# Kernel optimization log

Measured on AMD Instinct MI355X. Metric: run time of the kernel, lower is better.

## Reference

```python
import jax, jax.numpy as jnp
import numpy as np

V = 32000      # vocab
TMAX = 1024    # BLOCK_SIZE
D = 768        # N_EMBD
H = 12         # N_HEAD
L = 12         # N_LAYER
HS = D // H    # head_size
FF = 4 * D
B, T = 4, 1024


def setup_inputs() -> dict:
    key = jax.random.key(0)
    ks = iter(jax.random.split(key, 40))
    n = lambda shape: 0.02 * jax.random.normal(next(ks), shape, dtype=jnp.float32)
    return dict(
        idx=jax.random.randint(next(ks), (B, T), 0, V),
        targets=jax.random.randint(next(ks), (B, T), 0, V),
        tok_emb=n((V, D)),
        pos_emb=n((TMAX, D)),
        Wq=n((L, H, D, HS)), Wk=n((L, H, D, HS)), Wv=n((L, H, D, HS)),
        Wo=n((L, D, D)), bo=jnp.zeros((L, D)),
        W1=n((L, D, FF)), b1=jnp.zeros((L, FF)),
        W2=n((L, FF, D)), b2=jnp.zeros((L, D)),
        ln1_g=jnp.ones((L, D)), ln1_b=jnp.zeros((L, D)),
        ln2_g=jnp.ones((L, D)), ln2_b=jnp.zeros((L, D)),
        lnf_g=jnp.ones((D,)), lnf_b=jnp.zeros((D,)),
        Wlm=n((D, V)), blm=jnp.zeros((V,)),
    )


def _ln(x, g, b, eps=1e-5):
    m = x.mean(-1, keepdims=True)
    v = x.var(-1, keepdims=True)
    return (x - m) * jax.lax.rsqrt(v + eps) * g + b


def reference(idx, targets, tok_emb, pos_emb, Wq, Wk, Wv, Wo, bo,
              W1, b1, W2, b2, ln1_g, ln1_b, ln2_g, ln2_b, lnf_g, lnf_b,
              Wlm, blm):
    Bsz, Tt = idx.shape
    x = tok_emb[idx] + pos_emb[:Tt]                      # [B,T,D]
    causal = jnp.tril(jnp.ones((Tt, Tt), dtype=bool))     # [T,T]

    def layer(x, p):
        wq, wk, wv, wo, bob, w1, b1b, w2, b2b, g1, be1, g2, be2 = p
        h = _ln(x, g1, be1)
        q = jnp.einsum('btd,hdk->bhtk', h, wq)
        k = jnp.einsum('btd,hdk->bhtk', h, wk)
        v = jnp.einsum('btd,hdk->bhtk', h, wv)
        wei = jnp.einsum('bhtk,bhsk->bhts', q, k) * (HS ** -0.5)
        wei = jnp.where(causal, wei, -jnp.inf)
        wei = jax.nn.softmax(wei, axis=-1)                # dropout=0 in eval
        att = jnp.einsum('bhts,bhsk->bhtk', wei, v)
        att = att.transpose(0, 2, 1, 3).reshape(Bsz, Tt, H * HS)  # concat heads
        x = x + att @ wo + bob
        h2 = _ln(x, g2, be2)
        x = x + jax.nn.relu(h2 @ w1 + b1b) @ w2 + b2b
        return x, None

    x, _ = jax.lax.scan(layer, x,
                        (Wq, Wk, Wv, Wo, bo, W1, b1, W2, b2,
                         ln1_g, ln1_b, ln2_g, ln2_b))
    x = _ln(x, lnf_g, lnf_b)
    logits = x @ Wlm + blm                                # [B,T,V]
    lf = logits.reshape(Bsz * Tt, V)
    tf = targets.reshape(-1)
    logp = jax.nn.log_softmax(lf, axis=-1)
    loss = -jnp.take_along_axis(logp, tf[:, None], axis=1).mean()
    return lf, loss
```

## Files before the change

kernel.cpp:

```cpp
#include <hip/hip_runtime.h>

constexpr int C_B   = 4;
constexpr int C_T   = 1024;
constexpr int C_D   = 768;
constexpr int C_H   = 12;
constexpr int C_HS  = 64;
constexpr int C_FF  = 3072;
constexpr int C_V   = 32000;
constexpr int C_L   = 12;
constexpr int ROWS  = C_B * C_T;
constexpr int QKVN  = 3 * C_D;

typedef __bf16 bf16;
typedef __attribute__((ext_vector_type(8))) __bf16 bf16x8;
typedef __attribute__((ext_vector_type(4))) float  f32x4;
typedef __attribute__((ext_vector_type(4))) short  s16x4;

static __device__ __forceinline__ void gload16(const void* g, void* l) {
  __builtin_amdgcn_global_load_lds((const __attribute__((address_space(1))) void*)g,
                                   (__attribute__((address_space(3))) void*)l,
                                   16, 0, 0);
}

__global__ __launch_bounds__(256) void embed_kernel(const int* __restrict__ idx,
    const float* __restrict__ tok, const float* __restrict__ pos, float* __restrict__ x) {
  int gid = blockIdx.x * 256 + threadIdx.x;
  int row = gid / C_D, d = gid - row * C_D;
  int t = row & (C_T - 1);
  x[gid] = tok[(long)idx[row] * C_D + d] + pos[(long)t * C_D + d];
}

__global__ __launch_bounds__(256) void ln_kernel(const float* __restrict__ x,
    const float* __restrict__ g, const float* __restrict__ bb, long goff,
    bf16* __restrict__ out) {
  int row = blockIdx.x, tid = threadIdx.x;
  const float* xr = x + (long)row * C_D;
  float v0 = xr[tid], v1 = xr[tid + 256], v2 = xr[tid + 512];
  float s = v0 + v1 + v2;
  float s2 = v0 * v0 + v1 * v1 + v2 * v2;
#pragma unroll
  for (int off = 32; off > 0; off >>= 1) {
    s  += __shfl_down(s, off);
    s2 += __shfl_down(s2, off);
  }
  __shared__ float sm[4], sq[4];
  if ((tid & 63) == 0) { sm[tid >> 6] = s; sq[tid >> 6] = s2; }
  __syncthreads();
  s  = sm[0] + sm[1] + sm[2] + sm[3];
  s2 = sq[0] + sq[1] + sq[2] + sq[3];
  float mean = s * (1.f / C_D);
  float var  = s2 * (1.f / C_D) - mean * mean;
  float rstd = rsqrtf(var + 1e-5f);
  bf16* orow = out + (long)row * C_D;
  orow[tid]       = (bf16)((v0 - mean) * rstd * g[goff + tid]       + bb[goff + tid]);
  orow[tid + 256] = (bf16)((v1 - mean) * rstd * g[goff + tid + 256] + bb[goff + tid + 256]);
  orow[tid + 512] = (bf16)((v2 - mean) * rstd * g[goff + tid + 512] + bb[goff + tid + 512]);
}

__global__ __launch_bounds__(256) void transpose_kernel(const float* __restrict__ src,
    bf16* __restrict__ dst, int K, int N, long soff0, int ntn) {
  __shared__ bf16 tile[32][33];
  const float* s = src + soff0;
  int tn = blockIdx.x % ntn, tk = blockIdx.x / ntn;
  int c = threadIdx.x & 31, r = threadIdx.x >> 5;
#pragma unroll
  for (int it = 0; it < 4; ++it)
    tile[r + 8 * it][c] = (bf16)s[(long)(tk * 32 + r + 8 * it) * N + tn * 32 + c];
  __syncthreads();
#pragma unroll
  for (int it = 0; it < 4; ++it)
    dst[(long)(tn * 32 + r + 8 * it) * K + tk * 32 + c] = tile[c][r + 8 * it];
}

__global__ __launch_bounds__(256) void transpose_layer_kernel(
    const float* __restrict__ Wq, const float* __restrict__ Wk,
    const float* __restrict__ Wv, const float* __restrict__ Wo,
    const float* __restrict__ W1, const float* __restrict__ W2,
    bf16* __restrict__ wqkvt, bf16* __restrict__ wot,
    bf16* __restrict__ w1t, bf16* __restrict__ w2t, int l) {
  int bid = blockIdx.x;
  const float* src; bf16* dst; int K, N, ntn, t;
  if (bid < 1728) {
    int which = bid / 576, r = bid % 576, head = r / 48;
    t = r % 48;
    const float* W = which == 0 ? Wq : which == 1 ? Wk : Wv;
    src = W + (long)l * C_H * C_D * C_HS + (long)head * C_D * C_HS;
    dst = wqkvt + (long)which * C_D * C_D + (long)head * C_HS * C_D;
    K = C_D; N = C_HS; ntn = 2;
  } else if (bid < 2304) {
    t = bid - 1728; src = Wo + (long)l * C_D * C_D; dst = wot;
    K = C_D; N = C_D; ntn = 24;
  } else if (bid < 4608) {
    t = bid - 2304; src = W1 + (long)l * C_D * C_FF; dst = w1t;
    K = C_D; N = C_FF; ntn = 96;
  } else {
    t = bid - 4608; src = W2 + (long)l * C_FF * C_D; dst = w2t;
    K = C_FF; N = C_D; ntn = 24;
  }
  __shared__ bf16 tile[32][33];
  int tn = t % ntn, tk = t / ntn;
  int c = threadIdx.x & 31, r = threadIdx.x >> 5;
#pragma unroll
  for (int it = 0; it < 4; ++it)
    tile[r + 8 * it][c] = (bf16)src[(long)(tk * 32 + r + 8 * it) * N + tn * 32 + c];
  __syncthreads();
#pragma unroll
  for (int it = 0; it < 4; ++it)
    dst[(long)(tn * 32 + r + 8 * it) * K + tk * 32 + c] = tile[c][r + 8 * it];
}

template <int MODE>
__global__ __launch_bounds__(512) void gemm256(const bf16* __restrict__ A,
    const bf16* __restrict__ Bt, const float* __restrict__ bias, long boff,
    void* __restrict__ outp, int N, int K) {
  __shared__ __attribute__((aligned(16))) char smem[131072];
  int tid = threadIdx.x;
  int l = tid & 63, w = tid >> 6;
  int wm = w >> 2, wn = w & 3;
  int lg = l >> 4, lr = l & 15;

  int nwg = gridDim.x;
  int fid = blockIdx.x;
  int swz = (fid & 7) * (nwg >> 3) + (fid >> 3);
  long row0 = (long)(swz & 15) * 256;
  long col0 = (long)(swz >> 4) * 256;

  int Y0 = tid * 16, Y1 = 8192 + tid * 16;
  auto dec = [](int Y, int& R, int& C) {
    int s = Y >> 10, y = Y & 1023;
    int r15 = y >> 6, z = y & 63;
    int q = (z ^ ((r15 & 8) << 2)) >> 4;
    R = (s >> 1) * 16 + r15;
    C = (s & 1) * 32 + q * 8;
  };
  int R0, C0, R1, C1;
  dec(Y0, R0, C0);  dec(Y1, R1, C1);
  const bf16* Ab = A  + row0 * K;
  const bf16* Bb = Bt + col0 * K;

  auto stage = [&](int d, int kt) {
    char* bb = smem + d * 65536;
    long kc = (long)kt * 64;
    gload16(Ab + (long)R0 * K + kc + C0, bb + Y0);
    gload16(Ab + (long)R1 * K + kc + C1, bb + Y1);
    gload16(Ab + (long)(128 + R0) * K + kc + C0, bb + 16384 + Y0);
    gload16(Ab + (long)(128 + R1) * K + kc + C1, bb + 16384 + Y1);
    gload16(Bb + (long)R0 * K + kc + C0, bb + 32768 + Y0);
    gload16(Bb + (long)R1 * K + kc + C1, bb + 32768 + Y1);
    gload16(Bb + (long)(128 + R0) * K + kc + C0, bb + 49152 + Y0);
    gload16(Bb + (long)(128 + R1) * K + kc + C1, bb + 49152 + Y1);
  };

  f32x4 acc[8][4];
  const f32x4 fz = {0.f, 0.f, 0.f, 0.f};
#pragma unroll
  for (int mf = 0; mf < 8; ++mf)
#pragma unroll
    for (int nf = 0; nf < 4; ++nf) acc[mf][nf] = fz;

  int aoff = lr * 64 + ((lg * 16) ^ ((lr & 8) << 2));
  int nk = K >> 6;
  stage(0, 0);
  int d = 0;
  for (int kt = 0; kt < nk; ++kt) {
    __syncthreads();
    if (kt + 1 < nk) stage(d ^ 1, kt + 1);
    const char* aB = smem + d * 65536 + wm * 16384;
    const char* bB = smem + d * 65536 + 32768 + (wn >> 1) * 16384;
    bf16x8 bfrag[4][2];
#pragma unroll
    for (int nf = 0; nf < 4; ++nf)
#pragma unroll
      for (int k = 0; k < 2; ++k)
        bfrag[nf][k] = *(const bf16x8*)(bB + ((((wn & 1) * 4 + nf) * 2 + k) << 10) + aoff);
#pragma unroll
    for (int p = 0; p < 4; ++p) {
      bf16x8 af[2][2];
#pragma unroll
      for (int mi = 0; mi < 2; ++mi)
#pragma unroll
        for (int k = 0; k < 2; ++k)
          af[mi][k] = *(const bf16x8*)(aB + (((p * 2 + mi) * 2 + k) << 10) + aoff);
      __builtin_amdgcn_s_setprio(1);
#pragma unroll
      for (int mi = 0; mi < 2; ++mi)
#pragma unroll
        for (int nf = 0; nf < 4; ++nf)
#pragma unroll
          for (int k = 0; k < 2; ++k)
            acc[p * 2 + mi][nf] = __builtin_amdgcn_mfma_f32_16x16x32_bf16(
                af[mi][k], bfrag[nf][k], acc[p * 2 + mi][nf], 0, 0, 0);
      __builtin_amdgcn_s_setprio(0);
    }
    d ^= 1;
  }
  __syncthreads();

  if (MODE == 0 || MODE == 1) {
    bf16* lc = (bf16*)smem;
#pragma unroll
    for (int nf = 0; nf < 4; ++nf) {
      int col = wn * 64 + nf * 16 + lr;
      float bv = bias ? bias[boff + col0 + col] : 0.f;
#pragma unroll
      for (int mf = 0; mf < 8; ++mf) {
        int rb = wm * 128 + mf * 16 + lg * 4;
#pragma unroll
        for (int r = 0; r < 4; ++r) {
          float v = acc[mf][nf][r] + bv;
          if (MODE == 1) v = fmaxf(v, 0.f);
          lc[(rb + r) * 256 + col] = (bf16)v;
        }
      }
    }
    __syncthreads();
#pragma unroll
    for (int it = 0; it < 16; ++it) {
      int byte = it * 8192 + tid * 16;
      int rl = byte >> 9, cb = byte & 511;
      *(bf16x8*)((bf16*)outp + (row0 + rl) * N + col0 + (cb >> 1)) =
          *(const bf16x8*)(smem + byte);
    }
  } else {
#pragma unroll
    for (int h = 0; h < 2; ++h) {
      if (h) __syncthreads();
      if (wm == h) {
        float* lf = (float*)smem;
#pragma unroll
        for (int nf = 0; nf < 4; ++nf) {
          int col = wn * 64 + nf * 16 + lr;
          float bv = bias ? bias[boff + col0 + col] : 0.f;
#pragma unroll
          for (int mf = 0; mf < 8; ++mf) {
            int rb = mf * 16 + lg * 4;
#pragma unroll
            for (int r = 0; r < 4; ++r)
              lf[(rb + r) * 256 + col] = acc[mf][nf][r] + bv;
          }
        }
      }
      __syncthreads();
#pragma unroll
      for (int it = 0; it < 16; ++it) {
        int byte = it * 8192 + tid * 16;
        int rl = byte >> 10, cb = byte & 1023;
        *(f32x4*)((float*)outp + (row0 + h * 128 + rl) * N + col0 + (cb >> 2)) =
            *(const f32x4*)(smem + byte);
      }
    }
  }
}

template <int MODE>
__global__ __launch_bounds__(256) void gemm_bt(const bf16* __restrict__ A,
    const bf16* __restrict__ Bt, const float* __restrict__ bias, long boff,
    void* __restrict__ outp, float* __restrict__ resid, int N, int K) {
  __shared__ __attribute__((aligned(16))) char smem[32768];
  int tid = threadIdx.x;
  int l = tid & 63;
  int w = tid >> 6, wr = w >> 1, wc = w & 1;
  int lg = l >> 4, lr = l & 15;

  int nwg = gridDim.x;
  int fid = blockIdx.x;
  int swz = (fid & 7) * (nwg >> 3) + (fid >> 3);
  long row0 = (long)(swz & 31) * 128;
  long col0 = (long)(swz >> 5) * 128;

  const bf16* ga = A  + (row0 + (tid >> 2)) * K + (tid & 3) * 8;
  const bf16* gb = Bt + (col0 + (tid >> 2)) * K + (tid & 3) * 8;

  f32x4 acc[4][4];
  const f32x4 fz = {0.f, 0.f, 0.f, 0.f};
#pragma unroll
  for (int m = 0; m < 4; ++m)
#pragma unroll
    for (int n = 0; n < 4; ++n) acc[m][n] = fz;

  int nk = K >> 5;
  {
    bf16* la = (bf16*)smem + tid * 8;
    bf16* lb = (bf16*)(smem + 8192) + tid * 8;
    gload16(ga, la);  gload16(ga + (long)64 * K, la + 2048);
    gload16(gb, lb);  gload16(gb + (long)64 * K, lb + 2048);
    ga += 32; gb += 32;
  }
  int cur = 0;
  for (int t = 0; t < nk; ++t) {
    __syncthreads();
    if (t + 1 < nk) {
      char* bufb = smem + (cur ^ 1) * 16384;
      bf16* la = (bf16*)bufb + tid * 8;
      bf16* lb = (bf16*)(bufb + 8192) + tid * 8;
      gload16(ga, la);  gload16(ga + (long)64 * K, la + 2048);
      gload16(gb, lb);  gload16(gb + (long)64 * K, lb + 2048);
      ga += 32; gb += 32;
    }
    const bf16* cA = (const bf16*)(smem + cur * 16384);
    const bf16* cB = (const bf16*)(smem + cur * 16384 + 8192);
    bf16x8 af[4], bfr[4];
#pragma unroll
    for (int m = 0; m < 4; ++m)
      af[m] = *(const bf16x8*)(cA + (wr * 64 + m * 16 + lr) * 32 + lg * 8);
#pragma unroll
    for (int n = 0; n < 4; ++n)
      bfr[n] = *(const bf16x8*)(cB + (wc * 64 + n * 16 + lr) * 32 + lg * 8);
#pragma unroll
    for (int m = 0; m < 4; ++m)
#pragma unroll
      for (int n = 0; n < 4; ++n)
        acc[m][n] = __builtin_amdgcn_mfma_f32_16x16x32_bf16(af[m], bfr[n], acc[m][n], 0, 0, 0);
    cur ^= 1;
  }
  __syncthreads();

#pragma unroll
  for (int pair = 0; pair < 2; ++pair) {
    float* lcf = (float*)smem;
#pragma unroll
    for (int n = 0; n < 4; ++n) {
      int gcl = wc * 64 + n * 16 + lr;
      float bv = bias ? bias[boff + col0 + gcl] : 0.f;
#pragma unroll
      for (int mi = 0; mi < 2; ++mi) {
        int m = pair * 2 + mi;
        int rl = wr * 32 + mi * 16 + lg * 4;
#pragma unroll
        for (int r = 0; r < 4; ++r)
          lcf[(rl + r) * 128 + gcl] = acc[m][n][r] + bv;
      }
    }
    __syncthreads();
#pragma unroll
    for (int it = 0; it < 8; ++it) {
      int byte = it * 4096 + tid * 16;
      int rl = byte >> 9;
      int cb = byte & 511;
      long gr = row0 + (rl >> 5) * 64 + pair * 32 + ((rl >> 4) & 1) * 16 + (rl & 15);
      f32x4 v = *(const f32x4*)(smem + byte);
      if (MODE == 2) {
        f32x4 g = *(const f32x4*)(resid + gr * N + col0 + (cb >> 2));
        v += g;
        *(f32x4*)(resid + gr * N + col0 + (cb >> 2)) = v;
      } else {
        *(f32x4*)((float*)outp + gr * N + col0 + (cb >> 2)) = v;
      }
    }
    __syncthreads();
  }
}

#define TRRD(D, OFF) asm volatile("ds_read_b64_tr_b16 %0, %1 offset:" OFF \
                                  : "=v"(D) : "v"(trp))
__global__ __launch_bounds__(64) void attn_kernel(const bf16* __restrict__ qkv,
                                                  bf16* __restrict__ attout) {
  int fid = blockIdx.x;
  int swzb = (fid & 7) * 384 + (fid >> 3);
  int qt = swzb & 63;
  int bh = swzb >> 6;
  int b = bh / C_H, h = bh % C_H;
  int l = threadIdx.x;
  int lg = l >> 4, lr = l & 15;
  const bf16* base = qkv + (long)b * C_T * QKVN;

  const bf16* qp = base + (long)(qt * 16 + lr) * QKVN + h * C_HS;
  bf16x8 qf0 = *(const bf16x8*)(qp + lg * 8);
  bf16x8 qf1 = *(const bf16x8*)(qp + 32 + lg * 8);

  const f32x4 fz = {0.f, 0.f, 0.f, 0.f};
  f32x4 o[4] = {fz, fz, fz, fz};
  float m_run[4], l_run[4];
#pragma unroll
  for (int r = 0; r < 4; ++r) { m_run[r] = -1e30f; l_run[r] = 0.f; }

  __shared__ __attribute__((aligned(16))) bf16 p_lds[16][40];
  __shared__ __attribute__((aligned(16))) bf16 vt_sub[2048];

  unsigned trp = (unsigned)(unsigned long)
      ((const __attribute__((address_space(3))) char*)vt_sub + l * 8);

  int nkt = (qt * 16 + 15) / 32 + 1;
  for (int kt = 0; kt < nkt; ++kt) {
    int key0 = kt * 32;
    f32x4 sacc[2];
#pragma unroll
    for (int ss = 0; ss < 2; ++ss) {
      const bf16* kp = base + (long)(key0 + ss * 16 + lr) * QKVN + C_D + h * C_HS;
      bf16x8 kf0 = *(const bf16x8*)(kp + lg * 8);
      bf16x8 kf1 = *(const bf16x8*)(kp + 32 + lg * 8);
      f32x4 a = fz;
      a = __builtin_amdgcn_mfma_f32_16x16x32_bf16(qf0, kf0, a, 0, 0, 0);
      a = __builtin_amdgcn_mfma_f32_16x16x32_bf16(qf1, kf1, a, 0, 0, 0);
      sacc[ss] = a;
    }
#pragma unroll
    for (int r = 0; r < 4; ++r) {
      int qrow = qt * 16 + lg * 4 + r;
      bool u0 = (key0 + lr) <= qrow;
      bool u1 = (key0 + 16 + lr) <= qrow;
      float s0 = u0 ? sacc[0][r] * 0.125f : -1e30f;
      float s1 = u1 ? sacc[1][r] * 0.125f : -1e30f;
      float mr = fmaxf(s0, s1);
      mr = fmaxf(mr, __shfl_xor(mr, 1));
      mr = fmaxf(mr, __shfl_xor(mr, 2));
      mr = fmaxf(mr, __shfl_xor(mr, 4));
      mr = fmaxf(mr, __shfl_xor(mr, 8));
      float mnew = fmaxf(m_run[r], mr);
      float scale = __expf(m_run[r] - mnew);
      float p0 = u0 ? __expf(s0 - mnew) : 0.f;
      float p1 = u1 ? __expf(s1 - mnew) : 0.f;
      float rs = p0 + p1;
      rs += __shfl_xor(rs, 1);
      rs += __shfl_xor(rs, 2);
      rs += __shfl_xor(rs, 4);
      rs += __shfl_xor(rs, 8);
      l_run[r] = l_run[r] * scale + rs;
      m_run[r] = mnew;
      o[0][r] *= scale; o[1][r] *= scale; o[2][r] *= scale; o[3][r] *= scale;
      p_lds[lg * 4 + r][lr]      = (bf16)p0;
      p_lds[lg * 4 + r][16 + lr] = (bf16)p1;
    }
#pragma unroll
    for (int it = 0; it < 4; ++it) {
      int kl = it * 8 + (l >> 3);
      int d0 = (l & 7) * 8;
      bf16x8 vv = *(const bf16x8*)(base + (long)(key0 + kl) * QKVN + 2 * C_D + h * C_HS + d0);
      int ba = ((d0 >> 4) << 10) + (((kl >> 2) & 1) << 9) + ((kl >> 3) << 7)
             + ((kl & 3) << 5) + ((d0 & 15) << 1);
      *(bf16x8*)((char*)vt_sub + ba) = vv;
    }
    __syncthreads();
    s16x4 t0a, t0b, t1a, t1b, t2a, t2b, t3a, t3b;
    TRRD(t0a, "0");    TRRD(t0b, "512");
    TRRD(t1a, "1024"); TRRD(t1b, "1536");
    TRRD(t2a, "2048"); TRRD(t2b, "2560");
    TRRD(t3a, "3072"); TRRD(t3b, "3584");
    bf16x8 pf = *(const bf16x8*)(&p_lds[lr][lg * 8]);
    asm volatile("s_waitcnt lgkmcnt(0)" ::: "memory");
    __builtin_amdgcn_sched_barrier(0);
    union uu { short s[8]; bf16x8 v; };
    auto mk = [](s16x4 a, s16x4 bq) {
      uu u;
      u.s[0] = a[0]; u.s[1] = a[1]; u.s[2] = a[2]; u.s[3] = a[3];
      u.s[4] = bq[0]; u.s[5] = bq[1]; u.s[6] = bq[2]; u.s[7] = bq[3];
      return u.v;
    };
    o[0] = __builtin_amdgcn_mfma_f32_16x16x32_bf16(pf, mk(t0a, t0b), o[0], 0, 0, 0);
    o[1] = __builtin_amdgcn_mfma_f32_16x16x32_bf16(pf, mk(t1a, t1b), o[1], 0, 0, 0);
    o[2] = __builtin_amdgcn_mfma_f32_16x16x32_bf16(pf, mk(t2a, t2b), o[2], 0, 0, 0);
    o[3] = __builtin_amdgcn_mfma_f32_16x16x32_bf16(pf, mk(t3a, t3b), o[3], 0, 0, 0);
    __syncthreads();
  }
#pragma unroll
  for (int c = 0; c < 4; ++c)
#pragma unroll
    for (int r = 0; r < 4; ++r) {
      int qrow = qt * 16 + lg * 4 + r;
      attout[((long)b * C_T + qrow) * C_D + h * C_HS + c * 16 + lr] =
          (bf16)(o[c][r] / l_run[r]);
    }
}

__global__ __launch_bounds__(256) void loss_kernel(const float* __restrict__ logits,
    const int* __restrict__ targets, float* __restrict__ rowloss) {
  int row = blockIdx.x, tid = threadIdx.x;
  const float* lrow = logits + (long)row * C_V;
  float m = -1e30f, sum = 0.f;
  for (int i4 = tid * 4; i4 < C_V; i4 += 1024) {
    f32x4 v4 = *(const f32x4*)(lrow + i4);
#pragma unroll
    for (int j = 0; j < 4; ++j) {
      float v = v4[j];
      if (v > m) { sum *= __expf(m - v); m = v; }
      sum += __expf(v - m);
    }
  }
#pragma unroll
  for (int off = 32; off > 0; off >>= 1) {
    float mo = __shfl_down(m, off), so = __shfl_down(sum, off);
    float M = fmaxf(m, mo);
    sum = sum * __expf(m - M) + so * __expf(mo - M);
    m = M;
  }
  __shared__ float sm[4], ss[4];
  if ((tid & 63) == 0) { sm[tid >> 6] = m; ss[tid >> 6] = sum; }
  __syncthreads();
  if (tid == 0) {
    float M = sm[0], S = ss[0];
    for (int wv = 1; wv < 4; ++wv) {
      float M2 = fmaxf(M, sm[wv]);
      S = S * __expf(M - M2) + ss[wv] * __expf(sm[wv] - M2);
      M = M2;
    }
    float lt = lrow[targets[row]];
    rowloss[row] = -(lt - M - logf(S));
  }
}

__global__ __launch_bounds__(256) void loss_final(const float* __restrict__ rowloss,
                                                  float* __restrict__ out) {
  int tid = threadIdx.x;
  float s = 0.f;
  for (int i = tid; i < ROWS; i += 256) s += rowloss[i];
#pragma unroll
  for (int off = 32; off > 0; off >>= 1) s += __shfl_down(s, off);
  __shared__ float sm[4];
  if ((tid & 63) == 0) sm[tid >> 6] = s;
  __syncthreads();
  if (tid == 0) out[0] = (sm[0] + sm[1] + sm[2] + sm[3]) * (1.f / ROWS);
}

extern "C" void kernel_launch(void* const* d_in, const int* in_sizes, int n_in,
                              void* d_out, int out_size, void* d_ws, size_t ws_size,
                              hipStream_t stream) {
  (void)in_sizes; (void)n_in; (void)out_size; (void)ws_size;
  const int*   idx     = (const int*)  d_in[0];
  const int*   targets = (const int*)  d_in[1];
  const float* tok     = (const float*)d_in[2];
  const float* pos     = (const float*)d_in[3];
  const float* Wq      = (const float*)d_in[4];
  const float* Wk      = (const float*)d_in[5];
  const float* Wv      = (const float*)d_in[6];
  const float* Wo      = (const float*)d_in[7];
  const float* bo      = (const float*)d_in[8];
  const float* W1      = (const float*)d_in[9];
  const float* b1      = (const float*)d_in[10];
  const float* W2      = (const float*)d_in[11];
  const float* b2      = (const float*)d_in[12];
  const float* ln1g    = (const float*)d_in[13];
  const float* ln1b    = (const float*)d_in[14];
  const float* ln2g    = (const float*)d_in[15];
  const float* ln2b    = (const float*)d_in[16];
  const float* lnfg    = (const float*)d_in[17];
  const float* lnfb    = (const float*)d_in[18];
  const float* Wlm     = (const float*)d_in[19];
  const float* blm     = (const float*)d_in[20];

  char* p = (char*)d_ws;
  auto alloc = [&](size_t bytes) {
    char* r = p; p += (bytes + 255) & ~(size_t)255; return r;
  };
  float* x       = (float*)alloc((size_t)ROWS * C_D * 4);
  bf16*  h       = (bf16*) alloc((size_t)ROWS * C_D * 2);
  bf16*  qkv     = (bf16*) alloc((size_t)ROWS * QKVN * 2);
  bf16*  attout  = (bf16*) alloc((size_t)ROWS * C_D * 2);
  bf16*  ffbuf   = (bf16*) alloc((size_t)ROWS * C_FF * 2);
  bf16*  wqkvt   = (bf16*) alloc((size_t)QKVN * C_D * 2);
  bf16*  wot     = (bf16*) alloc((size_t)C_D * C_D * 2);
  bf16*  w1t     = (bf16*) alloc((size_t)C_FF * C_D * 2);
  bf16*  w2t     = (bf16*) alloc((size_t)C_D * C_FF * 2);
  float* rowloss = (float*)alloc((size_t)ROWS * 4);
  bf16*  wlmt    = qkv;

  float* logits = (float*)d_out;

  embed_kernel<<<ROWS * C_D / 256, 256, 0, stream>>>(idx, tok, pos, x);

  for (int l = 0; l < C_L; ++l) {
    transpose_layer_kernel<<<6912, 256, 0, stream>>>(
        Wq, Wk, Wv, Wo, W1, W2, wqkvt, wot, w1t, w2t, l);

    ln_kernel<<<ROWS, 256, 0, stream>>>(x, ln1g, ln1b, (long)l * C_D, h);
    gemm256<0><<<16 * (QKVN / 256), 512, 0, stream>>>(
        h, wqkvt, nullptr, 0, qkv, QKVN, C_D);
    attn_kernel<<<C_B * C_H * (C_T / 16), 64, 0, stream>>>(qkv, attout);
    gemm_bt<2><<<(C_D / 128) * 32, 256, 0, stream>>>(
        attout, wot, bo, (long)l * C_D, nullptr, x, C_D, C_D);
    ln_kernel<<<ROWS, 256, 0, stream>>>(x, ln2g, ln2b, (long)l * C_D, h);
    gemm256<1><<<16 * (C_FF / 256), 512, 0, stream>>>(
        h, w1t, b1, (long)l * C_FF, ffbuf, C_FF, C_D);
    gemm_bt<2><<<(C_D / 128) * 32, 256, 0, stream>>>(
        ffbuf, w2t, b2, (long)l * C_D, nullptr, x, C_D, C_FF);
  }

  transpose_kernel<<<(C_V / 32) * (C_D / 32), 256, 0, stream>>>(
      Wlm, wlmt, C_D, C_V, 0, C_V / 32);

  ln_kernel<<<ROWS, 256, 0, stream>>>(x, lnfg, lnfb, 0, h);
  gemm256<3><<<16 * (C_V / 256), 512, 0, stream>>>(
      h, wlmt, blm, 0, logits, C_V, C_D);
  loss_kernel<<<ROWS, 256, 0, stream>>>(logits, targets, rowloss);
  loss_final<<<1, 256, 0, stream>>>(rowloss, logits + (long)ROWS * C_V);
}
```

Before: 3.071 ms.

## Batch weight transposes, switch layer GEMMs to 128-tile kernel, fuse LM-head softmax partials

All layer weights and the LM head are now transposed to bf16 in a single upfront launch into per-layer buffers, replacing 12 per-layer transpose launches plus a separate LM-head transpose. QKV and FF1 GEMMs move from the 256-tile kernel to the 128-tile kernel with a new bf16 epilogue (ReLU fused for FF1), which gives more workgroups for these shapes. The LM-head GEMM epilogue now computes per-256-column online-softmax partials, so the loss kernel merges 125 partials per row instead of rereading the full logits. The costs are extra workspace and a small extra reduction buffer.

```diff
diff --git a/kernel.cpp b/kernel.cpp
--- a/kernel.cpp
+++ b/kernel.cpp
@@ -10,6 +10,7 @@
 constexpr int C_L   = 12;
 constexpr int ROWS  = C_B * C_T;
 constexpr int QKVN  = 3 * C_D;
+constexpr int NCB   = C_V / 256;
 
 typedef __bf16 bf16;
 typedef __attribute__((ext_vector_type(8))) __bf16 bf16x8;
@@ -57,45 +58,40 @@
   orow[tid + 512] = (bf16)((v2 - mean) * rstd * g[goff + tid + 512] + bb[goff + tid + 512]);
 }
 
-__global__ __launch_bounds__(256) void transpose_kernel(const float* __restrict__ src,
-    bf16* __restrict__ dst, int K, int N, long soff0, int ntn) {
-  __shared__ bf16 tile[32][33];
-  const float* s = src + soff0;
-  int tn = blockIdx.x % ntn, tk = blockIdx.x / ntn;
-  int c = threadIdx.x & 31, r = threadIdx.x >> 5;
-#pragma unroll
-  for (int it = 0; it < 4; ++it)
-    tile[r + 8 * it][c] = (bf16)s[(long)(tk * 32 + r + 8 * it) * N + tn * 32 + c];
-  __syncthreads();
-#pragma unroll
-  for (int it = 0; it < 4; ++it)
-    dst[(long)(tn * 32 + r + 8 * it) * K + tk * 32 + c] = tile[c][r + 8 * it];
-}
-
-__global__ __launch_bounds__(256) void transpose_layer_kernel(
+__global__ __launch_bounds__(256) void transpose_all_kernel(
     const float* __restrict__ Wq, const float* __restrict__ Wk,
     const float* __restrict__ Wv, const float* __restrict__ Wo,
     const float* __restrict__ W1, const float* __restrict__ W2,
+    const float* __restrict__ Wlm,
     bf16* __restrict__ wqkvt, bf16* __restrict__ wot,
-    bf16* __restrict__ w1t, bf16* __restrict__ w2t, int l) {
+    bf16* __restrict__ w1t, bf16* __restrict__ w2t, bf16* __restrict__ wlmt) {
   int bid = blockIdx.x;
   const float* src; bf16* dst; int K, N, ntn, t;
-  if (bid < 1728) {
-    int which = bid / 576, r = bid % 576, head = r / 48;
-    t = r % 48;
-    const float* W = which == 0 ? Wq : which == 1 ? Wk : Wv;
-    src = W + (long)l * C_H * C_D * C_HS + (long)head * C_D * C_HS;
-    dst = wqkvt + (long)which * C_D * C_D + (long)head * C_HS * C_D;
-    K = C_D; N = C_HS; ntn = 2;
-  } else if (bid < 2304) {
-    t = bid - 1728; src = Wo + (long)l * C_D * C_D; dst = wot;
-    K = C_D; N = C_D; ntn = 24;
-  } else if (bid < 4608) {
-    t = bid - 2304; src = W1 + (long)l * C_D * C_FF; dst = w1t;
-    K = C_D; N = C_FF; ntn = 96;
+  if (bid < 82944) {
+    int l = bid / 6912, sub = bid % 6912;
+    if (sub < 1728) {
+      int which = sub / 576, r = sub % 576, head = r / 48;
+      t = r % 48;
+      const float* W = which == 0 ? Wq : which == 1 ? Wk : Wv;
+      src = W + (long)l * C_H * C_D * C_HS + (long)head * C_D * C_HS;
+      dst = wqkvt + (long)l * QKVN * C_D + (long)which * C_D * C_D + (long)head * C_HS * C_D;
+      K = C_D; N = C_HS; ntn = 2;
+    } else if (sub < 2304) {
+      t = sub - 1728;
+      src = Wo + (long)l * C_D * C_D;  dst = wot + (long)l * C_D * C_D;
+      K = C_D; N = C_D; ntn = 24;
+    } else if (sub < 4608) {
+      t = sub - 2304;
+      src = W1 + (long)l * C_D * C_FF; dst = w1t + (long)l * C_FF * C_D;
+      K = C_D; N = C_FF; ntn = 96;
+    } else {
+      t = sub - 4608;
+      src = W2 + (long)l * C_FF * C_D; dst = w2t + (long)l * C_D * C_FF;
+      K = C_FF; N = C_D; ntn = 24;
+    }
   } else {
-    t = bid - 4608; src = W2 + (long)l * C_FF * C_D; dst = w2t;
-    K = C_FF; N = C_D; ntn = 24;
+    t = bid - 82944; src = Wlm; dst = wlmt;
+    K = C_D; N = C_V; ntn = C_V / 32;
   }
   __shared__ bf16 tile[32][33];
   int tn = t % ntn, tk = t / ntn;
@@ -112,7 +108,7 @@
 template <int MODE>
 __global__ __launch_bounds__(512) void gemm256(const bf16* __restrict__ A,
     const bf16* __restrict__ Bt, const float* __restrict__ bias, long boff,
-    void* __restrict__ outp, int N, int K) {
+    void* __restrict__ outp, float* __restrict__ lossp, int N, int K) {
   __shared__ __attribute__((aligned(16))) char smem[131072];
   int tid = threadIdx.x;
   int l = tid & 63, w = tid >> 6;
@@ -124,6 +120,7 @@
   int swz = (fid & 7) * (nwg >> 3) + (fid >> 3);
   long row0 = (long)(swz & 15) * 256;
   long col0 = (long)(swz >> 4) * 256;
+  int cbi = (int)(col0 >> 8);
 
   int Y0 = tid * 16, Y1 = 8192 + tid * 16;
   auto dec = [](int Y, int& R, int& C) {
@@ -248,6 +245,33 @@
         *(f32x4*)((float*)outp + (row0 + h * 128 + rl) * N + col0 + (cb >> 2)) =
             *(const f32x4*)(smem + byte);
       }
+      if (MODE == 3 && lossp) {
+        const float* lf = (const float*)smem;
+        int row = tid >> 2, chunk = tid & 3;
+        float M = -1e30f, S = 0.f;
+#pragma unroll
+        for (int j = 0; j < 16; ++j) {
+          int jj = (j + row) & 15;
+          f32x4 v = *(const f32x4*)(lf + row * 256 + chunk * 64 + jj * 4);
+#pragma unroll
+          for (int q = 0; q < 4; ++q) {
+            float xv = v[q];
+            if (xv > M) { S *= __expf(M - xv); M = xv; }
+            S += __expf(xv - M);
+          }
+        }
+#pragma unroll
+        for (int off = 1; off < 4; off <<= 1) {
+          float Mo = __shfl_xor(M, off), So = __shfl_xor(S, off);
+          float Mn = fmaxf(M, Mo);
+          S = S * __expf(M - Mn) + So * __expf(Mo - Mn);
+          M = Mn;
+        }
+        if (chunk == 0) {
+          long pi = ((row0 + h * 128 + row) * NCB + cbi) * 2;
+          lossp[pi] = M;  lossp[pi + 1] = S;
+        }
+      }
     }
   }
 }
@@ -315,39 +339,67 @@
   }
   __syncthreads();
 
-#pragma unroll
-  for (int pair = 0; pair < 2; ++pair) {
-    float* lcf = (float*)smem;
+  if (MODE == 0 || MODE == 1) {
+    bf16* lc = (bf16*)smem;
 #pragma unroll
     for (int n = 0; n < 4; ++n) {
       int gcl = wc * 64 + n * 16 + lr;
       float bv = bias ? bias[boff + col0 + gcl] : 0.f;
 #pragma unroll
-      for (int mi = 0; mi < 2; ++mi) {
-        int m = pair * 2 + mi;
-        int rl = wr * 32 + mi * 16 + lg * 4;
-#pragma unroll
-        for (int r = 0; r < 4; ++r)
-          lcf[(rl + r) * 128 + gcl] = acc[m][n][r] + bv;
+      for (int m = 0; m < 4; ++m) {
+        int rb = wr * 64 + m * 16 + lg * 4;
+#pragma unroll
+        for (int r = 0; r < 4; ++r) {
+          float v = acc[m][n][r] + bv;
+          if (MODE == 1) v = fmaxf(v, 0.f);
+          lc[(rb + r) * 128 + gcl] = (bf16)v;
+        }
       }
     }
     __syncthreads();
 #pragma unroll
     for (int it = 0; it < 8; ++it) {
       int byte = it * 4096 + tid * 16;
-      int rl = byte >> 9;
-      int cb = byte & 511;
-      long gr = row0 + (rl >> 5) * 64 + pair * 32 + ((rl >> 4) & 1) * 16 + (rl & 15);
-      f32x4 v = *(const f32x4*)(smem + byte);
-      if (MODE == 2) {
-        f32x4 g = *(const f32x4*)(resid + gr * N + col0 + (cb >> 2));
-        v += g;
-        *(f32x4*)(resid + gr * N + col0 + (cb >> 2)) = v;
-      } else {
-        *(f32x4*)((float*)outp + gr * N + col0 + (cb >> 2)) = v;
+      int rl = byte >> 8;
+      int cb = byte & 255;
+      *(bf16x8*)((bf16*)outp + (row0 + rl) * N + col0 + (cb >> 1)) =
+          *(const bf16x8*)(smem + byte);
+    }
+  } else {
+#pragma unroll
+    for (int pair = 0; pair < 2; ++pair) {
+      float* lcf = (float*)smem;
+#pragma unroll
+      for (int n = 0; n < 4; ++n) {
+        int gcl = wc * 64 + n * 16 + lr;
+        float bv = bias ? bias[boff + col0 + gcl] : 0.f;
+#pragma unroll
+        for (int mi = 0; mi < 2; ++mi) {
+          int m = pair * 2 + mi;
+          int rl = wr * 32 + mi * 16 + lg * 4;
+#pragma unroll
+          for (int r = 0; r < 4; ++r)
+            lcf[(rl + r) * 128 + gcl] = acc[m][n][r] + bv;
+        }
       }
-    }
-    __syncthreads();
+      __syncthreads();
+#pragma unroll
+      for (int it = 0; it < 8; ++it) {
+        int byte = it * 4096 + tid * 16;
+        int rl = byte >> 9;
+        int cb = byte & 511;
+        long gr = row0 + (rl >> 5) * 64 + pair * 32 + ((rl >> 4) & 1) * 16 + (rl & 15);
+        f32x4 v = *(const f32x4*)(smem + byte);
+        if (MODE == 2) {
+          f32x4 g = *(const f32x4*)(resid + gr * N + col0 + (cb >> 2));
+          v += g;
+          *(f32x4*)(resid + gr * N + col0 + (cb >> 2)) = v;
+        } else {
+          *(f32x4*)((float*)outp + gr * N + col0 + (cb >> 2)) = v;
+        }
+      }
+      __syncthreads();
+    }
   }
 }
 
@@ -462,40 +514,20 @@
     }
 }
 
-__global__ __launch_bounds__(256) void loss_kernel(const float* __restrict__ logits,
-    const int* __restrict__ targets, float* __restrict__ rowloss) {
-  int row = blockIdx.x, tid = threadIdx.x;
-  const float* lrow = logits + (long)row * C_V;
-  float m = -1e30f, sum = 0.f;
-  for (int i4 = tid * 4; i4 < C_V; i4 += 1024) {
-    f32x4 v4 = *(const f32x4*)(lrow + i4);
-#pragma unroll
-    for (int j = 0; j < 4; ++j) {
-      float v = v4[j];
-      if (v > m) { sum *= __expf(m - v); m = v; }
-      sum += __expf(v - m);
-    }
-  }
-#pragma unroll
-  for (int off = 32; off > 0; off >>= 1) {
-    float mo = __shfl_down(m, off), so = __shfl_down(sum, off);
-    float M = fmaxf(m, mo);
-    sum = sum * __expf(m - M) + so * __expf(mo - M);
-    m = M;
-  }
-  __shared__ float sm[4], ss[4];
-  if ((tid & 63) == 0) { sm[tid >> 6] = m; ss[tid >> 6] = sum; }
-  __syncthreads();
-  if (tid == 0) {
-    float M = sm[0], S = ss[0];
-    for (int wv = 1; wv < 4; ++wv) {
-      float M2 = fmaxf(M, sm[wv]);
-      S = S * __expf(M - M2) + ss[wv] * __expf(sm[wv] - M2);
-      M = M2;
-    }
-    float lt = lrow[targets[row]];
-    rowloss[row] = -(lt - M - logf(S));
-  }
+__global__ __launch_bounds__(128) void loss_partial_kernel(const float* __restrict__ lossp,
+    const float* __restrict__ logits, const int* __restrict__ targets,
+    float* __restrict__ rowloss) {
+  int row = blockIdx.x * 128 + threadIdx.x;
+  const float* pp = lossp + (long)row * NCB * 2;
+  float M = -1e30f, S = 0.f;
+  for (int i = 0; i < NCB; ++i) {
+    float pm = pp[i * 2], ps = pp[i * 2 + 1];
+    float Mn = fmaxf(M, pm);
+    S = S * __expf(M - Mn) + ps * __expf(pm - Mn);
+    M = Mn;
+  }
+  float lt = logits[(long)row * C_V + targets[row]];
+  rowloss[row] = -(lt - M - logf(S));
 }
 
 __global__ __launch_bounds__(256) void loss_final(const float* __restrict__ rowloss,
@@ -546,40 +578,37 @@
   bf16*  qkv     = (bf16*) alloc((size_t)ROWS * QKVN * 2);
   bf16*  attout  = (bf16*) alloc((size_t)ROWS * C_D * 2);
   bf16*  ffbuf   = (bf16*) alloc((size_t)ROWS * C_FF * 2);
-  bf16*  wqkvt   = (bf16*) alloc((size_t)QKVN * C_D * 2);
-  bf16*  wot     = (bf16*) alloc((size_t)C_D * C_D * 2);
-  bf16*  w1t     = (bf16*) alloc((size_t)C_FF * C_D * 2);
-  bf16*  w2t     = (bf16*) alloc((size_t)C_D * C_FF * 2);
+  bf16*  wqkvt   = (bf16*) alloc((size_t)C_L * QKVN * C_D * 2);
+  bf16*  wot     = (bf16*) alloc((size_t)C_L * C_D * C_D * 2);
+  bf16*  w1t     = (bf16*) alloc((size_t)C_L * C_FF * C_D * 2);
+  bf16*  w2t     = (bf16*) alloc((size_t)C_L * C_D * C_FF * 2);
+  bf16*  wlmt    = (bf16*) alloc((size_t)C_V * C_D * 2);
   float* rowloss = (float*)alloc((size_t)ROWS * 4);
-  bf16*  wlmt    = qkv;
+  float* lossp   = (float*)alloc((size_t)ROWS * NCB * 2 * 4);
 
   float* logits = (float*)d_out;
 
+  transpose_all_kernel<<<106944, 256, 0, stream>>>(
+      Wq, Wk, Wv, Wo, W1, W2, Wlm, wqkvt, wot, w1t, w2t, wlmt);
   embed_kernel<<<ROWS * C_D / 256, 256, 0, stream>>>(idx, tok, pos, x);
 
   for (int l = 0; l < C_L; ++l) {
-    transpose_layer_kernel<<<6912, 256, 0, stream>>>(
-        Wq, Wk, Wv, Wo, W1, W2, wqkvt, wot, w1t, w2t, l);
-
     ln_kernel<<<ROWS, 256, 0, stream>>>(x, ln1g, ln1b, (long)l * C_D, h);
-    gemm256<0><<<16 * (QKVN / 256), 512, 0, stream>>>(
-        h, wqkvt, nullptr, 0, qkv, QKVN, C_D);
+    gemm_bt<0><<<(QKVN / 128) * 32, 256, 0, stream>>>(
+        h, wqkvt + (long)l * QKVN * C_D, nullptr, 0, qkv, nullptr, QKVN, C_D);
     attn_kernel<<<C_B * C_H * (C_T / 16), 64, 0, stream>>>(qkv, attout);
     gemm_bt<2><<<(C_D / 128) * 32, 256, 0, stream>>>(
-        attout, wot, bo, (long)l * C_D, nullptr, x, C_D, C_D);
+        attout, wot + (long)l * C_D * C_D, bo, (long)l * C_D, nullptr, x, C_D, C_D);
     ln_kernel<<<ROWS, 256, 0, stream>>>(x, ln2g, ln2b, (long)l * C_D, h);
-    gemm256<1><<<16 * (C_FF / 256), 512, 0, stream>>>(
-        h, w1t, b1, (long)l * C_FF, ffbuf, C_FF, C_D);
+    gemm_bt<1><<<(C_FF / 128) * 32, 256, 0, stream>>>(
+        h, w1t + (long)l * C_FF * C_D, b1, (long)l * C_FF, ffbuf, nullptr, C_FF, C_D);
     gemm_bt<2><<<(C_D / 128) * 32, 256, 0, stream>>>(
-        ffbuf, w2t, b2, (long)l * C_D, nullptr, x, C_D, C_FF);
-  }
-
-  transpose_kernel<<<(C_V / 32) * (C_D / 32), 256, 0, stream>>>(
-      Wlm, wlmt, C_D, C_V, 0, C_V / 32);
+        ffbuf, w2t + (long)l * C_D * C_FF, b2, (long)l * C_D, nullptr, x, C_D, C_FF);
+  }
 
   ln_kernel<<<ROWS, 256, 0, stream>>>(x, lnfg, lnfb, 0, h);
   gemm256<3><<<16 * (C_V / 256), 512, 0, stream>>>(
-      h, wlmt, blm, 0, logits, C_V, C_D);
-  loss_kernel<<<ROWS, 256, 0, stream>>>(logits, targets, rowloss);
+      h, wlmt, blm, 0, logits, lossp, C_V, C_D);
+  loss_partial_kernel<<<ROWS / 128, 128, 0, stream>>>(lossp, logits, targets, rowloss);
   loss_final<<<1, 256, 0, stream>>>(rowloss, logits + (long)ROWS * C_V);
 }
```

Result: slower. 3.262 ms (+6.2%).
